# Performance work log

Measured on AMD Instinct MI355X. Metric: run time of the kernel, lower is better.

Reference implementation:

```python
import jax, jax.numpy as jnp
import numpy as np

B, T, V, H, E = 64, 64, 32000, 512, 256
EPS = 0.1
CLAMP_MIN = 1e-8


def setup_inputs() -> dict:
    key = jax.random.key(0)
    ks = jax.random.split(key, 7)
    s = 0.05  # small init scale to keep logits in a sane range
    return {
        "embedding": jax.random.normal(ks[0], (V, E), jnp.float32) * s,
        "w_ih": jax.random.normal(ks[1], (3 * H, E), jnp.float32) * s,
        "b_ih": jax.random.normal(ks[2], (3 * H,), jnp.float32) * s,
        "w_hh": jax.random.normal(ks[3], (3 * H, H), jnp.float32) * s,
        "b_hh": jax.random.normal(ks[4], (3 * H,), jnp.float32) * s,
        "w_out": jax.random.normal(ks[5], (V, H), jnp.float32) * s,
        "b_out": jax.random.normal(ks[6], (V,), jnp.float32) * s,
    }


def _gru_cell(x, h, w_ih, b_ih, w_hh, b_hh):
    # torch GRUCell: gates ordered (r, z, n)
    gi = x @ w_ih.T + b_ih          # [B, 3H]
    gh = h @ w_hh.T + b_hh          # [B, 3H]
    gi_r, gi_z, gi_n = jnp.split(gi, 3, axis=1)
    gh_r, gh_z, gh_n = jnp.split(gh, 3, axis=1)
    r = jax.nn.sigmoid(gi_r + gh_r)
    z = jax.nn.sigmoid(gi_z + gh_z)
    n = jnp.tanh(gi_n + r * gh_n)
    return (1.0 - z) * n + z * h


def reference(embedding, w_ih, b_ih, w_hh, b_hh, w_out, b_out):
    log_unif = -jnp.log(jnp.float32(V))

    def step(carry, key):
        hidden, inputs = carry
        hidden = _gru_cell(inputs, hidden, w_ih, b_ih, w_hh, b_hh)
        dist = jax.nn.log_softmax(hidden @ w_out.T + b_out, axis=-1)  # [B, V]
        dist_new = jax.lax.stop_gradient(dist)
        prob = jnp.exp(dist_new)
        prob_mean = prob.mean(0)  # [V]
        k_eps, k_gum = jax.random.split(key)
        # eps-sample: with prob EPS replace row with uniform log-prob
        draw = EPS >= jax.random.uniform(k_eps, (B,))
        dist_eps = jnp.where(draw[:, None], log_unif, dist_new)
        # Gumbel-max sampling
        u = jax.random.uniform(k_gum, (B, V), minval=1e-9, maxval=1.0)
        sampled = jnp.argmax(dist_eps - jnp.log(-jnp.log(u)), axis=1)  # [B]
        idx = sampled[:, None]
        logprob = jnp.take_along_axis(dist, idx, axis=1)[:, 0]
        onpolicy = jnp.clip(jnp.take_along_axis(prob, idx, axis=1)[:, 0], CLAMP_MIN, 1.0)
        offpolicy = jnp.clip(jnp.exp(jnp.take_along_axis(dist_eps, idx, axis=1)[:, 0]), CLAMP_MIN, 1.0)
        correction = onpolicy / offpolicy
        inputs_next = embedding[sampled]  # [B, E]
        return (hidden, inputs_next), (sampled, correction, logprob, dist, prob_mean)

    hidden0 = jnp.zeros((B, H), jnp.float32)
    inputs0 = jnp.broadcast_to(embedding[0], (B, E))  # embedding of zero token
    keys = jax.random.split(jax.random.key(1), T)
    _, (samples, corrections, logprobs, dists, probs) = jax.lax.scan(
        step, (hidden0, inputs0), keys)
    # scan stacks along time: transpose to batch-major like torch.cat(dim=1)
    return (samples.T,            # [B, T] int
            corrections.T,        # [B, T]
            logprobs.T,           # [B, T]
            dists.transpose(1, 0, 2),  # [B, T, V]
            probs)                # [T, V]
```

## Files before the change

### kernel.cpp

```cpp
#include <hip/hip_runtime.h>
#include <cstdint>
#include <cstddef>


#define JAX_PARTITIONABLE 1

#define Bn 64
#define Tn 64
#define Vn 32000
#define Hn 512
#define En 256

typedef unsigned short u16;
typedef __attribute__((ext_vector_type(8))) __bf16 bf16x8;
typedef __attribute__((ext_vector_type(4))) float f32x4;
typedef __attribute__((ext_vector_type(4))) uint32_t u32x4;

#define OUT_SAMP 0
#define OUT_CORR (Bn * Tn)
#define OUT_LOGP (2 * Bn * Tn)
#define OUT_DIST (3 * Bn * Tn)
#define OUT_PROB (3 * Bn * Tn + (size_t)Bn * Tn * Vn)

#define WS_H0   0
#define WS_H1   (Bn * Hn)
#define WS_G    (2 * Bn * Hn)
#define WS_GHN  (WS_G + Bn * 3 * Hn)
#define WS_RMAX (WS_GHN + Bn * Hn)
#define WS_RLSE (WS_RMAX + Bn)
#define WS_SMP  (WS_RLSE + Bn)
#define WS_HS0  (WS_SMP + Bn)
#define WS_HS1  (WS_HS0 + Bn * Hn / 2)
#define WS_HS2  (WS_HS1 + Bn * Hn / 2)
#define WS_PM   (WS_HS2 + Bn * Hn / 2)
#define WS_PS   (WS_PM + Vn)
#define WS_PBS  (WS_PS + Vn)
#define WS_PBV  (WS_PBS + Vn)
#define WS_PBZ  (WS_PBV + Vn)

__device__ __forceinline__ void tf2x32(uint32_t k0, uint32_t k1,
                                       uint32_t x0, uint32_t x1,
                                       uint32_t& o0, uint32_t& o1) {
  uint32_t ks2 = k0 ^ k1 ^ 0x1BD11BDAu;
  x0 += k0; x1 += k1;
#define TFR(r) { x0 += x1; x1 = (x1 << r) | (x1 >> (32 - r)); x1 ^= x0; }
  TFR(13) TFR(15) TFR(26) TFR(6)  x0 += k1;  x1 += ks2 + 1u;
  TFR(17) TFR(29) TFR(16) TFR(24) x0 += ks2; x1 += k0 + 2u;
  TFR(13) TFR(15) TFR(26) TFR(6)  x0 += k0;  x1 += k1 + 3u;
  TFR(17) TFR(29) TFR(16) TFR(24) x0 += k1;  x1 += ks2 + 4u;
  TFR(13) TFR(15) TFR(26) TFR(6)  x0 += ks2; x1 += k0 + 5u;
#undef TFR
  o0 = x0; o1 = x1;
}

__device__ __forceinline__ uint32_t jax_bits32(uint32_t k0, uint32_t k1,
                                               uint32_t i, uint32_t total) {
#if JAX_PARTITIONABLE
  (void)total;
  uint32_t o0, o1; tf2x32(k0, k1, 0u, i, o0, o1); return o0 ^ o1;
#else
  uint32_t half = total >> 1;
  uint32_t o0, o1;
  if (i < half) { tf2x32(k0, k1, i, i + half, o0, o1); return o0; }
  tf2x32(k0, k1, i - half, i, o0, o1); return o1;
#endif
}

__device__ __forceinline__ void jax_splitkey(uint32_t k0, uint32_t k1,
                                             uint32_t idx, uint32_t num,
                                             uint32_t& s0, uint32_t& s1) {
#if JAX_PARTITIONABLE
  (void)num;
  tf2x32(k0, k1, 0u, idx, s0, s1);
#else
  uint32_t j0 = 2 * idx, j1 = 2 * idx + 1;
  uint32_t r0, r1;
  if (j0 < num) { tf2x32(k0, k1, j0, j0 + num, r0, r1); s0 = r0; }
  else          { tf2x32(k0, k1, j0 - num, j0, r0, r1); s0 = r1; }
  if (j1 < num) { tf2x32(k0, k1, j1, j1 + num, r0, r1); s1 = r0; }
  else          { tf2x32(k0, k1, j1 - num, j1, r0, r1); s1 = r1; }
#endif
}

__device__ __forceinline__ float bits_to_unit(uint32_t bits) {
  return __uint_as_float((bits >> 9) | 0x3F800000u) - 1.0f;
}

struct Limbs3 { uint32_t p0, p1, p2; };

__device__ __forceinline__ Limbs3 split3_pair(float xa, float xb) {
  const uint32_t a0 = __float_as_uint(xa) & 0xFFFF0000u;
  const float ar1 = xa - __uint_as_float(a0);
  const uint32_t a1 = __float_as_uint(ar1) & 0xFFFF0000u;
  const float ar2 = ar1 - __uint_as_float(a1);
  const uint32_t a2 = __float_as_uint(ar2) & 0xFFFF0000u;
  const uint32_t b0 = __float_as_uint(xb) & 0xFFFF0000u;
  const float br1 = xb - __uint_as_float(b0);
  const uint32_t b1 = __float_as_uint(br1) & 0xFFFF0000u;
  const float br2 = br1 - __uint_as_float(b1);
  const uint32_t b2 = __float_as_uint(br2) & 0xFFFF0000u;
  Limbs3 r;
  r.p0 = (a0 >> 16) | b0;
  r.p1 = (a1 >> 16) | b1;
  r.p2 = (a2 >> 16) | b2;
  return r;
}


__global__ void init_k(float* h0, int* sampled) {
  int i = blockIdx.x * 256 + threadIdx.x;
  if (i < Bn * Hn) h0[i] = 0.0f;
  if (i < Bn) sampled[i] = 0;
}

__global__ void gru_gemm(const float* __restrict__ emb,
                         const float* __restrict__ w_ih, const float* __restrict__ b_ih,
                         const float* __restrict__ w_hh, const float* __restrict__ b_hh,
                         const float* __restrict__ h_prev, const int* __restrict__ sampled,
                         float* __restrict__ G, float* __restrict__ GHN) {
  const int blk = blockIdx.x;
  const bool isG = blk < 96;
  const int col0 = isG ? blk * 16 : (blk - 96) * 16;
  const int K = isG ? (En + Hn) : Hn;

  __shared__ float As[32][65];
  __shared__ float Bs[32][17];

  const int tid = threadIdx.x;
  const int tx = tid & 15;
  const int tyy = tid >> 4;
  float acc[4] = {0.f, 0.f, 0.f, 0.f};

  const int ab = tid >> 2;
  const int ak = (tid & 3) * 8;
  const int smp = sampled[ab];

  for (int k0 = 0; k0 < K; k0 += 32) {
    {
      const int kg = k0 + ak;
      const float* src;
      if (isG) src = (kg < En) ? (emb + (size_t)smp * En + kg)
                               : (h_prev + (size_t)ab * Hn + (kg - En));
      else     src = h_prev + (size_t)ab * Hn + kg;
      float4 v0 = *(const float4*)(src);
      float4 v1 = *(const float4*)(src + 4);
      As[ak + 0][ab] = v0.x; As[ak + 1][ab] = v0.y;
      As[ak + 2][ab] = v0.z; As[ak + 3][ab] = v0.w;
      As[ak + 4][ab] = v1.x; As[ak + 5][ab] = v1.y;
      As[ak + 6][ab] = v1.z; As[ak + 7][ab] = v1.w;
    }
    if (tid < 128) {
      const int c = tid >> 3;
      const int kk = (tid & 7) * 4;
      const int kg = k0 + kk;
      const int col = col0 + c;
      const float* src;
      if (isG) src = (kg < En) ? (w_ih + (size_t)col * En + kg)
                               : (w_hh + (size_t)col * Hn + (kg - En));
      else     src = w_hh + (size_t)(2 * Hn + col) * Hn + kg;
      float4 vv = *(const float4*)src;
      Bs[kk + 0][c] = vv.x; Bs[kk + 1][c] = vv.y;
      Bs[kk + 2][c] = vv.z; Bs[kk + 3][c] = vv.w;
    }
    __syncthreads();
#pragma unroll
    for (int k = 0; k < 32; k++) {
      const float w = Bs[k][tx];
#pragma unroll
      for (int i = 0; i < 4; i++) acc[i] = fmaf(As[k][tyy * 4 + i], w, acc[i]);
    }
    __syncthreads();
  }

  const int col = col0 + tx;
  if (isG) {
    const float bias = b_ih[col] + b_hh[col];
#pragma unroll
    for (int i = 0; i < 4; i++) {
      const int b = tyy * 4 + i;
      G[(size_t)b * (3 * Hn) + col] = acc[i] + bias;
    }
  } else {
    const float bias = b_hh[2 * Hn + col];
#pragma unroll
    for (int i = 0; i < 4; i++) {
      const int b = tyy * 4 + i;
      GHN[(size_t)b * Hn + col] = acc[i] + bias;
    }
  }
}

__global__ void gates_k(const float* __restrict__ G, const float* __restrict__ GHN,
                        const float* __restrict__ h_prev, float* __restrict__ h_new,
                        u16* __restrict__ hs0, u16* __restrict__ hs1,
                        u16* __restrict__ hs2) {
  const int idx = blockIdx.x * 256 + threadIdx.x;
  const int b = idx >> 9, j = idx & (Hn - 1);
  const float gr = G[(size_t)b * (3 * Hn) + j];
  const float gz = G[(size_t)b * (3 * Hn) + Hn + j];
  const float gn = G[(size_t)b * (3 * Hn) + 2 * Hn + j];
  const float ghn = GHN[(size_t)b * Hn + j];
  const float r = 1.0f / (1.0f + expf(-gr));
  const float z = 1.0f / (1.0f + expf(-gz));
  const float n = tanhf((gn - ghn) + r * ghn);
  const float hp = h_prev[(size_t)b * Hn + j];
  const float h = (1.0f - z) * n + z * hp;
  h_new[idx] = h;
  const uint32_t c0 = __float_as_uint(h) & 0xFFFF0000u;
  const float r1 = h - __uint_as_float(c0);
  const uint32_t c1 = __float_as_uint(r1) & 0xFFFF0000u;
  const float r2 = r1 - __uint_as_float(c1);
  hs0[idx] = (u16)(c0 >> 16);
  hs1[idx] = (u16)(c1 >> 16);
  hs2[idx] = (u16)(__float_as_uint(r2) >> 16);
}

__global__ __launch_bounds__(256, 2) void logits_mfma(
    const u16* __restrict__ hs0, const u16* __restrict__ hs1,
    const u16* __restrict__ hs2,
    const float* __restrict__ w_out, const float* __restrict__ b_out,
    float* __restrict__ out_dist,
    float* __restrict__ pM, float* __restrict__ pS, float* __restrict__ pBS,
    int* __restrict__ pBV, float* __restrict__ pBZ, int t) {
  const int tid = threadIdx.x;
  const int w = tid >> 6;
  const int lane = tid & 63;
  const int wm = (w >> 1) * 32;
  const int wn = (w & 1) * 32;
  const int lr = lane & 15;
  const int lg = lane >> 4;
  const int v0 = blockIdx.x * 64;

  __shared__ int s_dr[64];
  __shared__ float ldsM[64][2], ldsS[64][2], ldsBS[64][2], ldsBZ[64][2];
  __shared__ int ldsBV[64][2];

  uint32_t kt0, kt1, kg0, kg1;
  jax_splitkey(0u, 1u, (uint32_t)t, (uint32_t)Tn, kt0, kt1);
  jax_splitkey(kt0, kt1, 1u, 2u, kg0, kg1);
  if (tid < 64) {
    uint32_t ke0, ke1;
    jax_splitkey(kt0, kt1, 0u, 2u, ke0, ke1);
    const uint32_t eb = jax_bits32(ke0, ke1, (uint32_t)tid, (uint32_t)Bn);
    s_dr[tid] = (0.1f >= bits_to_unit(eb)) ? 1 : 0;
  }
  __syncthreads();

  f32x4 acc[2][2] = {};

#pragma unroll 2
  for (int k0 = 0; k0 < Hn; k0 += 32) {
    bf16x8 a0[2], a1[2], a2[2];
#pragma unroll
    for (int mi = 0; mi < 2; mi++) {
      const size_t off = (size_t)(wm + mi * 16 + lr) * Hn + k0 + lg * 8;
      a0[mi] = *reinterpret_cast<const bf16x8*>(hs0 + off);
      a1[mi] = *reinterpret_cast<const bf16x8*>(hs1 + off);
      a2[mi] = *reinterpret_cast<const bf16x8*>(hs2 + off);
    }
    bf16x8 bb0[2], bb1[2], bb2[2];
#pragma unroll
    for (int ni = 0; ni < 2; ni++) {
      const float* src = w_out + (size_t)(v0 + wn + ni * 16 + lr) * Hn + k0 + lg * 8;
      const float4 x0 = *(const float4*)(src);
      const float4 x1 = *(const float4*)(src + 4);
      u32x4 q0, q1, q2;
      const Limbs3 l0 = split3_pair(x0.x, x0.y);
      const Limbs3 l1 = split3_pair(x0.z, x0.w);
      const Limbs3 l2 = split3_pair(x1.x, x1.y);
      const Limbs3 l3 = split3_pair(x1.z, x1.w);
      q0[0] = l0.p0; q1[0] = l0.p1; q2[0] = l0.p2;
      q0[1] = l1.p0; q1[1] = l1.p1; q2[1] = l1.p2;
      q0[2] = l2.p0; q1[2] = l2.p1; q2[2] = l2.p2;
      q0[3] = l3.p0; q1[3] = l3.p1; q2[3] = l3.p2;
      bb0[ni] = __builtin_bit_cast(bf16x8, q0);
      bb1[ni] = __builtin_bit_cast(bf16x8, q1);
      bb2[ni] = __builtin_bit_cast(bf16x8, q2);
    }
#pragma unroll
    for (int mi = 0; mi < 2; mi++)
#pragma unroll
      for (int ni = 0; ni < 2; ni++) {
        f32x4 c = acc[mi][ni];
        c = __builtin_amdgcn_mfma_f32_16x16x32_bf16(a0[mi], bb0[ni], c, 0, 0, 0);
        c = __builtin_amdgcn_mfma_f32_16x16x32_bf16(a0[mi], bb1[ni], c, 0, 0, 0);
        c = __builtin_amdgcn_mfma_f32_16x16x32_bf16(a1[mi], bb0[ni], c, 0, 0, 0);
        c = __builtin_amdgcn_mfma_f32_16x16x32_bf16(a1[mi], bb1[ni], c, 0, 0, 0);
        c = __builtin_amdgcn_mfma_f32_16x16x32_bf16(a0[mi], bb2[ni], c, 0, 0, 0);
        c = __builtin_amdgcn_mfma_f32_16x16x32_bf16(a2[mi], bb0[ni], c, 0, 0, 0);
        acc[mi][ni] = c;
      }
  }

  float bias[2];
#pragma unroll
  for (int ni = 0; ni < 2; ni++) bias[ni] = b_out[v0 + wn + ni * 16 + lr];
#pragma unroll
  for (int mi = 0; mi < 2; mi++)
#pragma unroll
    for (int ni = 0; ni < 2; ni++)
#pragma unroll
      for (int r = 0; r < 4; r++) {
        acc[mi][ni][r] += bias[ni];
        const int brow = wm + mi * 16 + lg * 4 + r;
        out_dist[(size_t)(brow * Tn + t) * Vn + v0 + wn + ni * 16 + lr] =
            acc[mi][ni][r];
      }

  const float LU = -logf((float)Vn);
#pragma unroll
  for (int mi = 0; mi < 2; mi++) {
#pragma unroll
    for (int r = 0; r < 4; r++) {
      const int brow = wm + mi * 16 + lg * 4 + r;
      const int dr = s_dr[brow];
      const int vA = v0 + wn + lr, vB = vA + 16;
      const float zA = acc[mi][0][r], zB = acc[mi][1][r];
      float mz = fmaxf(zA, zB);
#pragma unroll
      for (int off = 1; off < 16; off <<= 1) mz = fmaxf(mz, __shfl_xor(mz, off, 64));
      float sz = expf(zA - mz) + expf(zB - mz);
#pragma unroll
      for (int off = 1; off < 16; off <<= 1) sz += __shfl_xor(sz, off, 64);
      const uint32_t bA = jax_bits32(kg0, kg1, (uint32_t)(brow * Vn + vA), 0u);
      const uint32_t bB = jax_bits32(kg0, kg1, (uint32_t)(brow * Vn + vB), 0u);
      const float uA = fmaxf(1e-9f, bits_to_unit(bA) + 1e-9f);
      const float uB = fmaxf(1e-9f, bits_to_unit(bB) + 1e-9f);
      const float glA = logf(-logf(uA));
      const float glB = logf(-logf(uB));
      const float sA = (dr ? LU : zA) - glA;
      const float sB = (dr ? LU : zB) - glB;
      float bs; int bv; float bz;
      if (sB > sA) { bs = sB; bv = vB; bz = zB; }
      else         { bs = sA; bv = vA; bz = zA; }
#pragma unroll
      for (int off = 1; off < 16; off <<= 1) {
        const float so = __shfl_xor(bs, off, 64);
        const int vo = __shfl_xor(bv, off, 64);
        const float zo = __shfl_xor(bz, off, 64);
        if (so > bs || (so == bs && vo < bv)) { bs = so; bv = vo; bz = zo; }
      }
      if (lr == 0) {
        ldsM[brow][w & 1] = mz; ldsS[brow][w & 1] = sz;
        ldsBS[brow][w & 1] = bs; ldsBV[brow][w & 1] = bv; ldsBZ[brow][w & 1] = bz;
      }
    }
  }
  __syncthreads();
  if (tid < 64) {
    const float m0 = ldsM[tid][0], m1 = ldsM[tid][1];
    const float mm = fmaxf(m0, m1);
    const float ss = ldsS[tid][0] * expf(m0 - mm) + ldsS[tid][1] * expf(m1 - mm);
    float bs = ldsBS[tid][0]; int bv = ldsBV[tid][0]; float bz = ldsBZ[tid][0];
    if (ldsBS[tid][1] > bs || (ldsBS[tid][1] == bs && ldsBV[tid][1] < bv)) {
      bs = ldsBS[tid][1]; bv = ldsBV[tid][1]; bz = ldsBZ[tid][1];
    }
    const int o = blockIdx.x * 64 + tid;
    pM[o] = mm; pS[o] = ss; pBS[o] = bs; pBV[o] = bv; pBZ[o] = bz;
  }
}

__global__ __launch_bounds__(256) void combine_k(
    const float* __restrict__ pM, const float* __restrict__ pS,
    const float* __restrict__ pBS, const int* __restrict__ pBV,
    const float* __restrict__ pBZ,
    float* __restrict__ rmax, float* __restrict__ rlse,
    int* __restrict__ sampled, float* __restrict__ out, int t) {
  const int row = blockIdx.x, tid = threadIdx.x;
  const int NB = Vn / 64;
  float mj[2] = {-INFINITY, -INFINITY}, sj[2] = {0.f, 0.f};
  float lbs = -INFINITY; int lbv = Vn; float lbz = 0.f;
#pragma unroll
  for (int q = 0; q < 2; q++) {
    const int j = tid + q * 256;
    if (j < NB) {
      const int o = j * 64 + row;
      mj[q] = pM[o]; sj[q] = pS[o];
      const float b = pBS[o]; const int v = pBV[o];
      if (b > lbs || (b == lbs && v < lbv)) { lbs = b; lbv = v; lbz = pBZ[o]; }
    }
  }
  __shared__ float rm[256], rs[256], rb[256], rz[256];
  __shared__ int rv[256];
  rm[tid] = fmaxf(mj[0], mj[1]); __syncthreads();
  for (int s = 128; s > 0; s >>= 1) {
    if (tid < s) rm[tid] = fmaxf(rm[tid], rm[tid + s]);
    __syncthreads();
  }
  const float mm = rm[0];
  float ls = 0.f;
#pragma unroll
  for (int q = 0; q < 2; q++)
    if (tid + q * 256 < NB) ls += sj[q] * expf(mj[q] - mm);
  rs[tid] = ls; rb[tid] = lbs; rv[tid] = lbv; rz[tid] = lbz; __syncthreads();
  for (int s = 128; s > 0; s >>= 1) {
    if (tid < s) {
      rs[tid] += rs[tid + s];
      if (rb[tid + s] > rb[tid] || (rb[tid + s] == rb[tid] && rv[tid + s] < rv[tid])) {
        rb[tid] = rb[tid + s]; rv[tid] = rv[tid + s]; rz[tid] = rz[tid + s];
      }
    }
    __syncthreads();
  }
  if (tid == 0) {
    const float l = logf(rs[0]);
    rmax[row] = mm; rlse[row] = l;
    const int v = rv[0];
    const float d = (rz[0] - mm) - l;
    sampled[row] = v;
    out[OUT_SAMP + row * Tn + t] = (float)v;
    out[OUT_LOGP + row * Tn + t] = d;
    uint32_t kt0, kt1, ke0, ke1;
    jax_splitkey(0u, 1u, (uint32_t)t, (uint32_t)Tn, kt0, kt1);
    jax_splitkey(kt0, kt1, 0u, 2u, ke0, ke1);
    const int dr =
        (0.1f >= bits_to_unit(jax_bits32(ke0, ke1, (uint32_t)row, (uint32_t)Bn)))
            ? 1 : 0;
    const float LU = -logf((float)Vn);
    const float onp = fminf(fmaxf(expf(d), 1e-8f), 1.0f);
    const float offp = fminf(fmaxf(expf(dr ? LU : d), 1e-8f), 1.0f);
    out[OUT_CORR + row * Tn + t] = onp / offp;
  }
}

__global__ void norm_probs_k(float* __restrict__ out_dist,
                             float* __restrict__ probs,
                             const float* __restrict__ rmax,
                             const float* __restrict__ rlse, int t) {
  __shared__ float sm[64], sl[64];
  const int tid = threadIdx.x;
  if (tid < 64) { sm[tid] = rmax[tid]; sl[tid] = rlse[tid]; }
  __syncthreads();
  const int v = blockIdx.x * 64 + (tid & 63);
  const int bq = tid >> 6;
  float s = 0.f;
#pragma unroll
  for (int i = 0; i < 16; i++) {
    const int b = bq * 16 + i;
    float* p = out_dist + (size_t)(b * Tn + t) * Vn + v;
    const float d = (*p - sm[b]) - sl[b];
    *p = d;
    s += expf(d);
  }
  __shared__ float red[256];
  red[tid] = s; __syncthreads();
  if (bq == 0)
    probs[(size_t)t * Vn + v] =
        (red[tid] + red[tid + 64] + red[tid + 128] + red[tid + 192]) * 0.015625f;
}

extern "C" void kernel_launch(void* const* d_in, const int* in_sizes, int n_in,
                              void* d_out, int out_size, void* d_ws, size_t ws_size,
                              hipStream_t stream) {
  const float* emb   = (const float*)d_in[0];
  const float* w_ih  = (const float*)d_in[1];
  const float* b_ih  = (const float*)d_in[2];
  const float* w_hh  = (const float*)d_in[3];
  const float* b_hh  = (const float*)d_in[4];
  const float* w_out = (const float*)d_in[5];
  const float* b_out = (const float*)d_in[6];
  float* out = (float*)d_out;
  float* ws  = (float*)d_ws;

  float* h_buf[2] = { ws + WS_H0, ws + WS_H1 };
  float* G    = ws + WS_G;
  float* GHN  = ws + WS_GHN;
  float* rmax = ws + WS_RMAX;
  float* rlse = ws + WS_RLSE;
  int*   smp  = (int*)(ws + WS_SMP);
  u16*   hs0  = (u16*)(ws + WS_HS0);
  u16*   hs1  = (u16*)(ws + WS_HS1);
  u16*   hs2  = (u16*)(ws + WS_HS2);
  float* pM   = ws + WS_PM;
  float* pS   = ws + WS_PS;
  float* pBS  = ws + WS_PBS;
  int*   pBV  = (int*)(ws + WS_PBV);
  float* pBZ  = ws + WS_PBZ;

  init_k<<<(Bn * Hn + 255) / 256, 256, 0, stream>>>(h_buf[0], smp);

  for (int t = 0; t < Tn; t++) {
    float* hp = h_buf[t & 1];
    float* hn = h_buf[(t + 1) & 1];
    gru_gemm<<<128, 256, 0, stream>>>(emb, w_ih, b_ih, w_hh, b_hh, hp, smp, G, GHN);
    gates_k<<<(Bn * Hn) / 256, 256, 0, stream>>>(G, GHN, hp, hn, hs0, hs1, hs2);
    logits_mfma<<<Vn / 64, 256, 0, stream>>>(hs0, hs1, hs2, w_out, b_out,
                                             out + OUT_DIST, pM, pS, pBS, pBV, pBZ, t);
    combine_k<<<Bn, 256, 0, stream>>>(pM, pS, pBS, pBV, pBZ, rmax, rlse, smp, out, t);
    norm_probs_k<<<Vn / 64, 256, 0, stream>>>(out + OUT_DIST, out + OUT_PROB,
                                              rmax, rlse, t);
  }
}
```

Before: 6.921 ms.

## Fuse GRU gates into GEMM, fold row combine into logits, defer normalization

Merges the GRU matmul and gate kernels into one kernel that keeps the hidden state transposed and splits K across waves. The per-row softmax/argmax combine moves into the logits kernel: an atomic ticket counter lets the last 8 blocks spin until all strips have written their partials, then reduce 8 rows each. Per-step log-softmax normalization and the prob-mean are deferred to a single kernel after the time loop, using per-timestep max and logsumexp arrays. The intent is to cut per-step launches from five to two and shorten the serial chain. The cost is spin-wait synchronization that depends on all blocks making progress, plus GRU weight reads that are no longer tiled through shared memory.

```diff
diff --git a/kernel.cpp b/kernel.cpp
--- a/kernel.cpp
+++ b/kernel.cpp
@@ -11,6 +11,9 @@
 #define Hn 512
 #define En 256
 
+#define NSTRIP 500
+#define SPAD   512
+
 typedef unsigned short u16;
 typedef __attribute__((ext_vector_type(8))) __bf16 bf16x8;
 typedef __attribute__((ext_vector_type(4))) float f32x4;
@@ -22,21 +25,20 @@
 #define OUT_DIST (3 * Bn * Tn)
 #define OUT_PROB (3 * Bn * Tn + (size_t)Bn * Tn * Vn)
 
-#define WS_H0   0
-#define WS_H1   (Bn * Hn)
-#define WS_G    (2 * Bn * Hn)
-#define WS_GHN  (WS_G + Bn * 3 * Hn)
-#define WS_RMAX (WS_GHN + Bn * Hn)
-#define WS_RLSE (WS_RMAX + Bn)
-#define WS_SMP  (WS_RLSE + Bn)
-#define WS_HS0  (WS_SMP + Bn)
+#define WS_HT0  0
+#define WS_HT1  (WS_HT0 + Hn * Bn)
+#define WS_RM   (WS_HT1 + Hn * Bn)
+#define WS_RL   (WS_RM + Tn * Bn)
+#define WS_SMP  (WS_RL + Tn * Bn)
+#define WS_CNT  (WS_SMP + Bn)
+#define WS_HS0  (WS_CNT + Bn)
 #define WS_HS1  (WS_HS0 + Bn * Hn / 2)
 #define WS_HS2  (WS_HS1 + Bn * Hn / 2)
 #define WS_PM   (WS_HS2 + Bn * Hn / 2)
-#define WS_PS   (WS_PM + Vn)
-#define WS_PBS  (WS_PS + Vn)
-#define WS_PBV  (WS_PBS + Vn)
-#define WS_PBZ  (WS_PBV + Vn)
+#define WS_PS   (WS_PM + Bn * SPAD)
+#define WS_PBS  (WS_PS + Bn * SPAD)
+#define WS_PBV  (WS_PBS + Bn * SPAD)
+#define WS_PBZ  (WS_PBV + Bn * SPAD)
 
 __device__ __forceinline__ void tf2x32(uint32_t k0, uint32_t k1,
                                        uint32_t x0, uint32_t x1,
@@ -107,112 +109,98 @@
 }
 
 
-__global__ void init_k(float* h0, int* sampled) {
+__global__ void init_k(float* h0, int* sampled, int* cnt) {
   int i = blockIdx.x * 256 + threadIdx.x;
   if (i < Bn * Hn) h0[i] = 0.0f;
-  if (i < Bn) sampled[i] = 0;
-}
-
-__global__ void gru_gemm(const float* __restrict__ emb,
-                         const float* __restrict__ w_ih, const float* __restrict__ b_ih,
-                         const float* __restrict__ w_hh, const float* __restrict__ b_hh,
-                         const float* __restrict__ h_prev, const int* __restrict__ sampled,
-                         float* __restrict__ G, float* __restrict__ GHN) {
-  const int blk = blockIdx.x;
-  const bool isG = blk < 96;
-  const int col0 = isG ? blk * 16 : (blk - 96) * 16;
-  const int K = isG ? (En + Hn) : Hn;
-
-  __shared__ float As[32][65];
-  __shared__ float Bs[32][17];
-
+  if (i < Bn) { sampled[i] = 0; cnt[i] = 0; }
+}
+
+__global__ __launch_bounds__(256) void gru_fused(
+    const float* __restrict__ emb,
+    const float* __restrict__ w_ih, const float* __restrict__ b_ih,
+    const float* __restrict__ w_hh, const float* __restrict__ b_hh,
+    const float* __restrict__ hT_prev, float* __restrict__ hT_new,
+    const int* __restrict__ sampled,
+    u16* __restrict__ hs0, u16* __restrict__ hs1, u16* __restrict__ hs2) {
   const int tid = threadIdx.x;
-  const int tx = tid & 15;
-  const int tyy = tid >> 4;
-  float acc[4] = {0.f, 0.f, 0.f, 0.f};
-
-  const int ab = tid >> 2;
-  const int ak = (tid & 3) * 8;
-  const int smp = sampled[ab];
-
-  for (int k0 = 0; k0 < K; k0 += 32) {
-    {
-      const int kg = k0 + ak;
-      const float* src;
-      if (isG) src = (kg < En) ? (emb + (size_t)smp * En + kg)
-                               : (h_prev + (size_t)ab * Hn + (kg - En));
-      else     src = h_prev + (size_t)ab * Hn + kg;
-      float4 v0 = *(const float4*)(src);
-      float4 v1 = *(const float4*)(src + 4);
-      As[ak + 0][ab] = v0.x; As[ak + 1][ab] = v0.y;
-      As[ak + 2][ab] = v0.z; As[ak + 3][ab] = v0.w;
-      As[ak + 4][ab] = v1.x; As[ak + 5][ab] = v1.y;
-      As[ak + 6][ab] = v1.z; As[ak + 7][ab] = v1.w;
-    }
-    if (tid < 128) {
-      const int c = tid >> 3;
-      const int kk = (tid & 7) * 4;
-      const int kg = k0 + kk;
-      const int col = col0 + c;
-      const float* src;
-      if (isG) src = (kg < En) ? (w_ih + (size_t)col * En + kg)
-                               : (w_hh + (size_t)col * Hn + (kg - En));
-      else     src = w_hh + (size_t)(2 * Hn + col) * Hn + kg;
-      float4 vv = *(const float4*)src;
-      Bs[kk + 0][c] = vv.x; Bs[kk + 1][c] = vv.y;
-      Bs[kk + 2][c] = vv.z; Bs[kk + 3][c] = vv.w;
-    }
-    __syncthreads();
-#pragma unroll
-    for (int k = 0; k < 32; k++) {
-      const float w = Bs[k][tx];
-#pragma unroll
-      for (int i = 0; i < 4; i++) acc[i] = fmaf(As[k][tyy * 4 + i], w, acc[i]);
-    }
-    __syncthreads();
-  }
-
-  const int col = col0 + tx;
-  if (isG) {
-    const float bias = b_ih[col] + b_hh[col];
-#pragma unroll
-    for (int i = 0; i < 4; i++) {
-      const int b = tyy * 4 + i;
-      G[(size_t)b * (3 * Hn) + col] = acc[i] + bias;
-    }
-  } else {
-    const float bias = b_hh[2 * Hn + col];
-#pragma unroll
-    for (int i = 0; i < 4; i++) {
-      const int b = tyy * 4 + i;
-      GHN[(size_t)b * Hn + col] = acc[i] + bias;
-    }
-  }
-}
-
-__global__ void gates_k(const float* __restrict__ G, const float* __restrict__ GHN,
-                        const float* __restrict__ h_prev, float* __restrict__ h_new,
-                        u16* __restrict__ hs0, u16* __restrict__ hs1,
-                        u16* __restrict__ hs2) {
-  const int idx = blockIdx.x * 256 + threadIdx.x;
-  const int b = idx >> 9, j = idx & (Hn - 1);
-  const float gr = G[(size_t)b * (3 * Hn) + j];
-  const float gz = G[(size_t)b * (3 * Hn) + Hn + j];
-  const float gn = G[(size_t)b * (3 * Hn) + 2 * Hn + j];
-  const float ghn = GHN[(size_t)b * Hn + j];
-  const float r = 1.0f / (1.0f + expf(-gr));
-  const float z = 1.0f / (1.0f + expf(-gz));
-  const float n = tanhf((gn - ghn) + r * ghn);
-  const float hp = h_prev[(size_t)b * Hn + j];
-  const float h = (1.0f - z) * n + z * hp;
-  h_new[idx] = h;
-  const uint32_t c0 = __float_as_uint(h) & 0xFFFF0000u;
-  const float r1 = h - __uint_as_float(c0);
-  const uint32_t c1 = __float_as_uint(r1) & 0xFFFF0000u;
-  const float r2 = r1 - __uint_as_float(c1);
-  hs0[idx] = (u16)(c0 >> 16);
-  hs1[idx] = (u16)(c1 >> 16);
-  hs2[idx] = (u16)(__float_as_uint(r2) >> 16);
+  const int b = tid & 63;
+  const int w = __builtin_amdgcn_readfirstlane(tid >> 6);
+  const int q = w & 1;
+  const int kh = w >> 1;
+  const int j = blockIdx.x * 2 + q;
+
+  __shared__ float Xs[En][64];
+  {
+    const int g = tid >> 6;
+    const float* src = emb + (size_t)sampled[b] * En + g * 64;
+#pragma unroll
+    for (int kk = 0; kk < 64; kk += 4) {
+      float4 v = *(const float4*)(src + kk);
+      Xs[g * 64 + kk + 0][b] = v.x;
+      Xs[g * 64 + kk + 1][b] = v.y;
+      Xs[g * 64 + kk + 2][b] = v.z;
+      Xs[g * 64 + kk + 3][b] = v.w;
+    }
+  }
+  __syncthreads();
+
+  float a_r = 0.f, a_z = 0.f, a_n = 0.f;
+  float g_r = 0.f, g_z = 0.f, g_n = 0.f;
+
+  {
+    const float* wr = w_ih + (size_t)j * En;
+    const float* wz = w_ih + (size_t)(Hn + j) * En;
+    const float* wn = w_ih + (size_t)(2 * Hn + j) * En;
+    const int kb = kh * 128;
+#pragma unroll 8
+    for (int k = kb; k < kb + 128; k++) {
+      const float xv = Xs[k][b];
+      a_r = fmaf(xv, wr[k], a_r);
+      a_z = fmaf(xv, wz[k], a_z);
+      a_n = fmaf(xv, wn[k], a_n);
+    }
+  }
+  {
+    const float* wr = w_hh + (size_t)j * Hn;
+    const float* wz = w_hh + (size_t)(Hn + j) * Hn;
+    const float* wn = w_hh + (size_t)(2 * Hn + j) * Hn;
+    const int kb = kh * 256;
+#pragma unroll 8
+    for (int k = kb; k < kb + 256; k++) {
+      const float hv = hT_prev[k * 64 + b];
+      g_r = fmaf(hv, wr[k], g_r);
+      g_z = fmaf(hv, wz[k], g_z);
+      g_n = fmaf(hv, wn[k], g_n);
+    }
+  }
+
+  __shared__ float red[6][2][64];
+  if (kh == 1) {
+    red[0][q][b] = a_r; red[1][q][b] = a_z; red[2][q][b] = a_n;
+    red[3][q][b] = g_r; red[4][q][b] = g_z; red[5][q][b] = g_n;
+  }
+  __syncthreads();
+  if (kh == 0) {
+    a_r += red[0][q][b]; a_z += red[1][q][b]; a_n += red[2][q][b];
+    g_r += red[3][q][b]; g_z += red[4][q][b]; g_n += red[5][q][b];
+    const float gr = a_r + b_ih[j] + g_r + b_hh[j];
+    const float gz = a_z + b_ih[Hn + j] + g_z + b_hh[Hn + j];
+    const float r = 1.0f / (1.0f + expf(-gr));
+    const float z = 1.0f / (1.0f + expf(-gz));
+    const float ghn = g_n + b_hh[2 * Hn + j];
+    const float n = tanhf(a_n + b_ih[2 * Hn + j] + r * ghn);
+    const float hp = hT_prev[j * 64 + b];
+    const float h = (1.0f - z) * n + z * hp;
+    hT_new[j * 64 + b] = h;
+    const uint32_t c0 = __float_as_uint(h) & 0xFFFF0000u;
+    const float r1 = h - __uint_as_float(c0);
+    const uint32_t c1 = __float_as_uint(r1) & 0xFFFF0000u;
+    const float r2 = r1 - __uint_as_float(c1);
+    const size_t ho = (size_t)b * Hn + j;
+    hs0[ho] = (u16)(c0 >> 16);
+    hs1[ho] = (u16)(c1 >> 16);
+    hs2[ho] = (u16)(__float_as_uint(r2) >> 16);
+  }
 }
 
 __global__ __launch_bounds__(256, 2) void logits_mfma(
@@ -221,7 +209,9 @@
     const float* __restrict__ w_out, const float* __restrict__ b_out,
     float* __restrict__ out_dist,
     float* __restrict__ pM, float* __restrict__ pS, float* __restrict__ pBS,
-    int* __restrict__ pBV, float* __restrict__ pBZ, int t) {
+    int* __restrict__ pBV, float* __restrict__ pBZ,
+    int* __restrict__ cnt, float* __restrict__ rmA, float* __restrict__ rlA,
+    int* __restrict__ sampled, float* __restrict__ out, int t) {
   const int tid = threadIdx.x;
   const int w = tid >> 6;
   const int lane = tid & 63;
@@ -234,6 +224,7 @@
   __shared__ int s_dr[64];
   __shared__ float ldsM[64][2], ldsS[64][2], ldsBS[64][2], ldsBZ[64][2];
   __shared__ int ldsBV[64][2];
+  __shared__ int s_tk;
 
   uint32_t kt0, kt1, kg0, kg1;
   jax_splitkey(0u, 1u, (uint32_t)t, (uint32_t)Tn, kt0, kt1);
@@ -355,88 +346,85 @@
     if (ldsBS[tid][1] > bs || (ldsBS[tid][1] == bs && ldsBV[tid][1] < bv)) {
       bs = ldsBS[tid][1]; bv = ldsBV[tid][1]; bz = ldsBZ[tid][1];
     }
-    const int o = blockIdx.x * 64 + tid;
+    const int o = tid * SPAD + blockIdx.x;
     pM[o] = mm; pS[o] = ss; pBS[o] = bs; pBV[o] = bv; pBZ[o] = bz;
   }
-}
-
-__global__ __launch_bounds__(256) void combine_k(
-    const float* __restrict__ pM, const float* __restrict__ pS,
-    const float* __restrict__ pBS, const int* __restrict__ pBV,
-    const float* __restrict__ pBZ,
-    float* __restrict__ rmax, float* __restrict__ rlse,
-    int* __restrict__ sampled, float* __restrict__ out, int t) {
-  const int row = blockIdx.x, tid = threadIdx.x;
-  const int NB = Vn / 64;
-  float mj[2] = {-INFINITY, -INFINITY}, sj[2] = {0.f, 0.f};
-  float lbs = -INFINITY; int lbv = Vn; float lbz = 0.f;
-#pragma unroll
-  for (int q = 0; q < 2; q++) {
-    const int j = tid + q * 256;
-    if (j < NB) {
-      const int o = j * 64 + row;
-      mj[q] = pM[o]; sj[q] = pS[o];
-      const float b = pBS[o]; const int v = pBV[o];
-      if (b > lbs || (b == lbs && v < lbv)) { lbs = b; lbv = v; lbz = pBZ[o]; }
-    }
-  }
-  __shared__ float rm[256], rs[256], rb[256], rz[256];
-  __shared__ int rv[256];
-  rm[tid] = fmaxf(mj[0], mj[1]); __syncthreads();
-  for (int s = 128; s > 0; s >>= 1) {
-    if (tid < s) rm[tid] = fmaxf(rm[tid], rm[tid + s]);
-    __syncthreads();
-  }
-  const float mm = rm[0];
-  float ls = 0.f;
-#pragma unroll
-  for (int q = 0; q < 2; q++)
-    if (tid + q * 256 < NB) ls += sj[q] * expf(mj[q] - mm);
-  rs[tid] = ls; rb[tid] = lbs; rv[tid] = lbv; rz[tid] = lbz; __syncthreads();
-  for (int s = 128; s > 0; s >>= 1) {
-    if (tid < s) {
-      rs[tid] += rs[tid + s];
-      if (rb[tid + s] > rb[tid] || (rb[tid + s] == rb[tid] && rv[tid + s] < rv[tid])) {
-        rb[tid] = rb[tid + s]; rv[tid] = rv[tid + s]; rz[tid] = rz[tid + s];
-      }
-    }
-    __syncthreads();
-  }
+  __syncthreads();
+
   if (tid == 0) {
-    const float l = logf(rs[0]);
-    rmax[row] = mm; rlse[row] = l;
-    const int v = rv[0];
-    const float d = (rz[0] - mm) - l;
-    sampled[row] = v;
-    out[OUT_SAMP + row * Tn + t] = (float)v;
-    out[OUT_LOGP + row * Tn + t] = d;
-    uint32_t kt0, kt1, ke0, ke1;
-    jax_splitkey(0u, 1u, (uint32_t)t, (uint32_t)Tn, kt0, kt1);
-    jax_splitkey(kt0, kt1, 0u, 2u, ke0, ke1);
-    const int dr =
-        (0.1f >= bits_to_unit(jax_bits32(ke0, ke1, (uint32_t)row, (uint32_t)Bn)))
-            ? 1 : 0;
-    const float LU = -logf((float)Vn);
-    const float onp = fminf(fmaxf(expf(d), 1e-8f), 1.0f);
-    const float offp = fminf(fmaxf(expf(dr ? LU : d), 1e-8f), 1.0f);
-    out[OUT_CORR + row * Tn + t] = onp / offp;
-  }
-}
-
-__global__ void norm_probs_k(float* __restrict__ out_dist,
-                             float* __restrict__ probs,
-                             const float* __restrict__ rmax,
-                             const float* __restrict__ rlse, int t) {
+    __threadfence();
+    s_tk = __hip_atomic_fetch_add(&cnt[t], 1, __ATOMIC_ACQ_REL,
+                                  __HIP_MEMORY_SCOPE_AGENT);
+  }
+  __syncthreads();
+  const int ticket = s_tk;
+  if (ticket >= NSTRIP - 8 && ticket < NSTRIP) {
+    while (__hip_atomic_load(&cnt[t], __ATOMIC_ACQUIRE,
+                             __HIP_MEMORY_SCOPE_AGENT) < NSTRIP) {
+      __builtin_amdgcn_s_sleep(8);
+    }
+    const int base = (ticket - (NSTRIP - 8)) * 8;
+    const int g = tid >> 5, l32 = tid & 31;
+    const int row = base + g;
+    float m = -INFINITY, ssum = 0.f;
+    float bs = -INFINITY; int bv = Vn; float bz = 0.f;
+    for (int s = l32; s < NSTRIP; s += 32) {
+      const int o = row * SPAD + s;
+      const float m2 = pM[o], s2 = pS[o];
+      const float mn = fmaxf(m, m2);
+      ssum = ssum * expf(m - mn) + s2 * expf(m2 - mn);
+      m = mn;
+      const float b2 = pBS[o]; const int v2 = pBV[o];
+      if (b2 > bs || (b2 == bs && v2 < bv)) { bs = b2; bv = v2; bz = pBZ[o]; }
+    }
+#pragma unroll
+    for (int off = 16; off >= 1; off >>= 1) {
+      const float mo = __shfl_xor(m, off, 64);
+      const float so = __shfl_xor(ssum, off, 64);
+      const float mn = fmaxf(m, mo);
+      ssum = ssum * expf(m - mn) + so * expf(mo - mn);
+      m = mn;
+      const float bo = __shfl_xor(bs, off, 64);
+      const int vo = __shfl_xor(bv, off, 64);
+      const float zo = __shfl_xor(bz, off, 64);
+      if (bo > bs || (bo == bs && vo < bv)) { bs = bo; bv = vo; bz = zo; }
+    }
+    if (l32 == 0) {
+      const float l = logf(ssum);
+      rmA[t * Bn + row] = m;
+      rlA[t * Bn + row] = l;
+      sampled[row] = bv;
+      out[OUT_SAMP + row * Tn + t] = (float)bv;
+      const float d = (bz - m) - l;
+      out[OUT_LOGP + row * Tn + t] = d;
+      uint32_t ke0, ke1;
+      jax_splitkey(kt0, kt1, 0u, 2u, ke0, ke1);
+      const int dr =
+          (0.1f >= bits_to_unit(jax_bits32(ke0, ke1, (uint32_t)row, (uint32_t)Bn)))
+              ? 1 : 0;
+      const float onp = fminf(fmaxf(expf(d), 1e-8f), 1.0f);
+      const float offp = fminf(fmaxf(expf(dr ? LU : d), 1e-8f), 1.0f);
+      out[OUT_CORR + row * Tn + t] = onp / offp;
+    }
+  }
+}
+
+__global__ void norm_all_k(float* __restrict__ out_dist,
+                           float* __restrict__ probs,
+                           const float* __restrict__ rmA,
+                           const float* __restrict__ rlA) {
+  const int blk = blockIdx.x;
+  const int t = blk / 250;
+  const int c = blk % 250;
+  const int tid = threadIdx.x;
+  const int v = c * 128 + (tid & 127);
+  const int half = tid >> 7;
   __shared__ float sm[64], sl[64];
-  const int tid = threadIdx.x;
-  if (tid < 64) { sm[tid] = rmax[tid]; sl[tid] = rlse[tid]; }
-  __syncthreads();
-  const int v = blockIdx.x * 64 + (tid & 63);
-  const int bq = tid >> 6;
+  if (tid < 64) { sm[tid] = rmA[t * Bn + tid]; sl[tid] = rlA[t * Bn + tid]; }
+  __syncthreads();
   float s = 0.f;
-#pragma unroll
-  for (int i = 0; i < 16; i++) {
-    const int b = bq * 16 + i;
+  for (int i = 0; i < 32; i++) {
+    const int b = half * 32 + i;
     float* p = out_dist + (size_t)(b * Tn + t) * Vn + v;
     const float d = (*p - sm[b]) - sl[b];
     *p = d;
@@ -444,9 +432,8 @@
   }
   __shared__ float red[256];
   red[tid] = s; __syncthreads();
-  if (bq == 0)
-    probs[(size_t)t * Vn + v] =
-        (red[tid] + red[tid + 64] + red[tid + 128] + red[tid + 192]) * 0.015625f;
+  if (half == 0)
+    probs[(size_t)t * Vn + v] = (red[tid] + red[tid + 128]) * 0.015625f;
 }
 
 extern "C" void kernel_launch(void* const* d_in, const int* in_sizes, int n_in,
@@ -462,12 +449,11 @@
   float* out = (float*)d_out;
   float* ws  = (float*)d_ws;
 
-  float* h_buf[2] = { ws + WS_H0, ws + WS_H1 };
-  float* G    = ws + WS_G;
-  float* GHN  = ws + WS_GHN;
-  float* rmax = ws + WS_RMAX;
-  float* rlse = ws + WS_RLSE;
+  float* hT[2] = { ws + WS_HT0, ws + WS_HT1 };
+  float* rmA  = ws + WS_RM;
+  float* rlA  = ws + WS_RL;
   int*   smp  = (int*)(ws + WS_SMP);
+  int*   cnt  = (int*)(ws + WS_CNT);
   u16*   hs0  = (u16*)(ws + WS_HS0);
   u16*   hs1  = (u16*)(ws + WS_HS1);
   u16*   hs2  = (u16*)(ws + WS_HS2);
@@ -477,17 +463,17 @@
   int*   pBV  = (int*)(ws + WS_PBV);
   float* pBZ  = ws + WS_PBZ;
 
-  init_k<<<(Bn * Hn + 255) / 256, 256, 0, stream>>>(h_buf[0], smp);
+  init_k<<<(Bn * Hn + 255) / 256, 256, 0, stream>>>(hT[0], smp, cnt);
 
   for (int t = 0; t < Tn; t++) {
-    float* hp = h_buf[t & 1];
-    float* hn = h_buf[(t + 1) & 1];
-    gru_gemm<<<128, 256, 0, stream>>>(emb, w_ih, b_ih, w_hh, b_hh, hp, smp, G, GHN);
-    gates_k<<<(Bn * Hn) / 256, 256, 0, stream>>>(G, GHN, hp, hn, hs0, hs1, hs2);
-    logits_mfma<<<Vn / 64, 256, 0, stream>>>(hs0, hs1, hs2, w_out, b_out,
-                                             out + OUT_DIST, pM, pS, pBS, pBV, pBZ, t);
-    combine_k<<<Bn, 256, 0, stream>>>(pM, pS, pBS, pBV, pBZ, rmax, rlse, smp, out, t);
-    norm_probs_k<<<Vn / 64, 256, 0, stream>>>(out + OUT_DIST, out + OUT_PROB,
-                                              rmax, rlse, t);
-  }
-}
+    float* hp = hT[t & 1];
+    float* hn = hT[(t + 1) & 1];
+    gru_fused<<<Hn / 2, 256, 0, stream>>>(emb, w_ih, b_ih, w_hh, b_hh,
+                                          hp, hn, smp, hs0, hs1, hs2);
+    logits_mfma<<<NSTRIP, 256, 0, stream>>>(hs0, hs1, hs2, w_out, b_out,
+                                            out + OUT_DIST, pM, pS, pBS, pBV, pBZ,
+                                            cnt, rmA, rlA, smp, out, t);
+  }
+  norm_all_k<<<Tn * 250, 256, 0, stream>>>(out + OUT_DIST, out + OUT_PROB,
+                                           rmA, rlA);
+}
```

After: 8.088 ms. 16.9% more time.
